# Performance work log

Hardware: AMD Instinct MI355X
Metric: run time of the kernel (lower is better)

Reference implementation:

```python
import jax, jax.numpy as jnp
import numpy as np

B, L, DM, DS, DC, E = 2, 1024, 1024, 16, 4, 2
DI = E * DM          # d_inner = 2048
DR = DM // 16        # dt_rank = 64
EPS = 1e-5


def setup_inputs() -> dict:
    key = jax.random.key(0)
    ks = jax.random.split(key, 8)
    s = lambda k, shp, sc: jax.random.normal(k, shp, jnp.float32) * sc
    return {
        "x": s(ks[0], (B, L, DM), 1.0),
        "norm_w": jnp.ones((DM,), jnp.float32),
        "in_proj_w": s(ks[1], (2 * DI, DM), 0.02),
        "conv_w": s(ks[2], (DI, 1, DC), 0.1),        # depthwise kernel [O=DI, I=1, W=DC]
        "conv_b": s(ks[3], (DI,), 0.02),
        "x_proj_w": s(ks[4], (DR + 2 * DS, DI), 0.02),
        "dt_proj_w": s(ks[5], (DI, DR), 0.02),
        "dt_proj_b": s(ks[6], (DI,), 0.02),
        "A_log": jnp.log(jnp.broadcast_to(jnp.arange(1, DS + 1, dtype=jnp.float32), (DI, DS))),
        "D": jnp.ones((DI,), jnp.float32),
        "out_proj_w": s(ks[7], (DM, DI), 0.02),
    }


def reference(x, norm_w, in_proj_w, conv_w, conv_b, x_proj_w,
              dt_proj_w, dt_proj_b, A_log, D, out_proj_w):
    # RMSNorm
    u = x * jax.lax.rsqrt(jnp.mean(x * x, axis=-1, keepdims=True) + EPS) * norm_w

    # in_proj -> [B, L, 2*DI], split into ssm branch and gate
    xz = jnp.einsum('bld,ed->ble', u, in_proj_w)
    xin, z = jnp.split(xz, 2, axis=-1)

    # causal depthwise conv along L + SiLU
    xc = jnp.transpose(xin, (0, 2, 1))                      # [B, DI, L]
    xc = jnp.pad(xc, ((0, 0), (0, 0), (DC - 1, 0)))
    xc = jax.lax.conv_general_dilated(xc, conv_w, (1,), 'VALID',
                                      feature_group_count=DI)  # [B, DI, L]
    xc = jax.nn.silu(xc + conv_b[None, :, None])
    xc = jnp.transpose(xc, (0, 2, 1))                       # [B, L, DI]

    # input-dependent dt, B, C
    dbl = jnp.einsum('bld,ed->ble', xc, x_proj_w)           # [B, L, DR+2*DS]
    dt, Bm, Cm = jnp.split(dbl, [DR, DR + DS], axis=-1)
    delta = jax.nn.softplus(jnp.einsum('blr,dr->bld', dt, dt_proj_w) + dt_proj_b)  # [B,L,DI]

    A = -jnp.exp(A_log)                                     # [DI, DS]
    dA = jnp.exp(delta[..., None] * A)                      # [B, L, DI, DS]
    dBu = delta[..., None] * Bm[:, :, None, :] * xc[..., None]  # [B, L, DI, DS]

    # selective scan: h_t = dA_t * h_{t-1} + dBu_t ; y_t = <h_t, C_t>
    def step(h, inp):
        da, dbu, c = inp
        h = da * h + dbu                                    # [B, DI, DS]
        return h, jnp.einsum('bdn,bn->bd', h, c)

    h0 = jnp.zeros((B, DI, DS), x.dtype)
    _, ys = jax.lax.scan(step, h0,
                         (jnp.swapaxes(dA, 0, 1),
                          jnp.swapaxes(dBu, 0, 1),
                          jnp.swapaxes(Cm, 0, 1)))
    y = jnp.swapaxes(ys, 0, 1) + xc * D                     # [B, L, DI]

    out = jnp.einsum('bld,ed->ble', y * jax.nn.silu(z), out_proj_w)
    return out + x  # residual
```

## Files before the change

### kernel.cpp

```cpp
#include <hip/hip_runtime.h>
#include <math.h>

#define B_   2
#define L_   1024
#define DM   1024
#define DS   16
#define DC   4
#define DI   2048
#define DR   64
#define NTOK (B_*L_)
#define EPSF 1e-5f
#define NC   32
#define CL   (L_/NC)
#define SPLITS 8

typedef __bf16 bf16_t;
typedef bf16_t bf16x4 __attribute__((ext_vector_type(4)));
typedef bf16_t bf16x8 __attribute__((ext_vector_type(8)));
typedef float  f32x4  __attribute__((ext_vector_type(4)));

__device__ __forceinline__ float siluf(float x){ return x / (1.f + __expf(-x)); }
__device__ __forceinline__ float softplusf(float x){ return (x > 20.f) ? x : log1pf(__expf(x)); }

__device__ __forceinline__ void gload_lds16(const void* g, void* l) {
    __builtin_amdgcn_global_load_lds(
        (const __attribute__((address_space(1))) void*)g,
        (__attribute__((address_space(3))) void*)l, 16, 0, 0);
}

struct hl_t { bf16_t h, l; };
__device__ __forceinline__ hl_t split2(float v) {
    hl_t r;
    r.h = (bf16_t)v;
    r.l = (bf16_t)(v - (float)r.h);
    return r;
}

#define SPLIT_IN_BLKS  ((2*DI*DM/4)/256)
#define SPLIT_X_BLKS   ((128*DI/4)/256)
#define SPLIT_O_BLKS   ((DM*DI/4)/256)
__global__ __launch_bounds__(256) void rms_split_all(
    const float* __restrict__ x, const float* __restrict__ w,
    bf16_t* __restrict__ uh, bf16_t* __restrict__ ul,
    const float* __restrict__ in_w, bf16_t* __restrict__ wih, bf16_t* __restrict__ wil,
    const float* __restrict__ x_w,  bf16_t* __restrict__ wxh,  bf16_t* __restrict__ wxl,
    const float* __restrict__ out_w, bf16_t* __restrict__ woh, bf16_t* __restrict__ wol)
{
    __shared__ float sred[4];
    int blk = blockIdx.x;
    int t = threadIdx.x;

    if (blk < NTOK) {
        int row = blk;
        float4 v = ((const float4*)(x + (size_t)row*DM))[t];
        float ss = v.x*v.x + v.y*v.y + v.z*v.z + v.w*v.w;
        #pragma unroll
        for (int off = 32; off > 0; off >>= 1) ss += __shfl_xor(ss, off, 64);
        if ((t & 63) == 0) sred[t >> 6] = ss;
        __syncthreads();
        ss = sred[0] + sred[1] + sred[2] + sred[3];
        float rs = rsqrtf(ss * (1.f/(float)DM) + EPSF);
        float4 wv = ((const float4*)w)[t];
        float o[4];
        o[0] = v.x*rs*wv.x; o[1] = v.y*rs*wv.y; o[2] = v.z*rs*wv.z; o[3] = v.w*rs*wv.w;
        bf16x4 hv, lv;
        #pragma unroll
        for (int j = 0; j < 4; ++j) { hl_t s = split2(o[j]); hv[j] = s.h; lv[j] = s.l; }
        *(bf16x4*)(uh + (size_t)row*DM + t*4) = hv;
        *(bf16x4*)(ul + (size_t)row*DM + t*4) = lv;
        return;
    }
    blk -= NTOK;
    if (blk < SPLIT_IN_BLKS) {
        int i = blk * 256 + t;
        float4 v = ((const float4*)in_w)[i];
        float o[4] = {v.x, v.y, v.z, v.w};
        bf16x4 hv, lv;
        #pragma unroll
        for (int j = 0; j < 4; ++j) { hl_t s = split2(o[j]); hv[j] = s.h; lv[j] = s.l; }
        ((bf16x4*)wih)[i] = hv;
        ((bf16x4*)wil)[i] = lv;
        return;
    }
    blk -= SPLIT_IN_BLKS;
    if (blk < SPLIT_X_BLKS) {
        int i = blk * 256 + t;
        int row = i >> 9;
        bf16x4 hv, lv;
        if (row < 96) {
            float4 v = ((const float4*)x_w)[i];
            float o[4] = {v.x, v.y, v.z, v.w};
            #pragma unroll
            for (int j = 0; j < 4; ++j) { hl_t s = split2(o[j]); hv[j] = s.h; lv[j] = s.l; }
        } else {
            #pragma unroll
            for (int j = 0; j < 4; ++j) { hv[j] = (bf16_t)0.f; lv[j] = (bf16_t)0.f; }
        }
        ((bf16x4*)wxh)[i] = hv;
        ((bf16x4*)wxl)[i] = lv;
        return;
    }
    blk -= SPLIT_X_BLKS;
    {
        int i = blk * 256 + t;
        float4 v = ((const float4*)out_w)[i];
        float o[4] = {v.x, v.y, v.z, v.w};
        bf16x4 hv, lv;
        #pragma unroll
        for (int j = 0; j < 4; ++j) { hl_t s = split2(o[j]); hv[j] = s.h; lv[j] = s.l; }
        ((bf16x4*)woh)[i] = hv;
        ((bf16x4*)wol)[i] = lv;
    }
}

template<int BN, int EPI, bool SK>
__global__ __launch_bounds__(256) void gemm_mfma(
    const bf16_t* __restrict__ Ah, const bf16_t* __restrict__ Al,
    const bf16_t* __restrict__ Bh, const bf16_t* __restrict__ Bl,
    float* __restrict__ C, int ldc,
    const float* __restrict__ res,
    int M, int N, int K, int kspl)
{
    constexpr int NJ   = BN / 32;
    constexpr int WN   = BN / 2;
    constexpr int ACH  = 8;
    constexpr int BCH  = BN / 16;
    constexpr int NCH  = 2*ACH + 2*BCH;
    constexpr int PERW = NCH / 4;
    constexpr int AOFF_L = 128*32;
    constexpr int BOFF_H = 2*128*32;
    constexpr int BOFF_L = 2*128*32 + BN*32;
    constexpr int BUFSZ  = 2*128*32 + 2*BN*32;

    __shared__ bf16_t lds[2*BUFSZ];

    int t = threadIdx.x;
    int w = t >> 6, lane = t & 63;
    int wr = w >> 1, wc = w & 1;

    int bx, by;
    if (!SK) {
        int bid = blockIdx.y * gridDim.x + blockIdx.x;
        int xcd = bid & 7;
        int i   = bid >> 3;
        bx = xcd * (int)(gridDim.x >> 3) + (i >> 4);
        by = i & 15;
    } else { bx = blockIdx.x; by = blockIdx.y; }

    int m0 = by * 128;
    int n0 = SK ? 0 : bx * BN;
    int k0beg = SK ? bx * kspl : 0;
    int nst = (SK ? kspl : K) >> 5;
    float* Cp = C;
    if (SK) Cp += (size_t)bx * M * BN;

    f32x4 acc[4][NJ];
    #pragma unroll
    for (int i = 0; i < 4; ++i)
        #pragma unroll
        for (int j = 0; j < NJ; ++j)
            acc[i][j] = (f32x4){0.f, 0.f, 0.f, 0.f};

    int lrow = lane >> 2;
    int lcol = (lane & 3) * 8;
    int ar   = wr*64 + (lane & 15);
    int br   = wc*WN + (lane & 15);
    int koff = (lane >> 4) * 8;

    auto STAGE = [&](int buf, int k0) {
        int base = buf ? BUFSZ : 0;
        #pragma unroll
        for (int q = 0; q < PERW; ++q) {
            int ch = w * PERW + q;
            const bf16_t* g; int le;
            if (ch < ACH) {
                int cc = ch;
                g  = Ah + (size_t)(m0 + cc*16 + lrow)*K + k0 + lcol;
                le = cc*512 + lane*8;
            } else if (ch < 2*ACH) {
                int cc = ch - ACH;
                g  = Al + (size_t)(m0 + cc*16 + lrow)*K + k0 + lcol;
                le = AOFF_L + cc*512 + lane*8;
            } else if (ch < 2*ACH + BCH) {
                int cc = ch - 2*ACH;
                g  = Bh + (size_t)(n0 + cc*16 + lrow)*K + k0 + lcol;
                le = BOFF_H + cc*512 + lane*8;
            } else {
                int cc = ch - 2*ACH - BCH;
                g  = Bl + (size_t)(n0 + cc*16 + lrow)*K + k0 + lcol;
                le = BOFF_L + cc*512 + lane*8;
            }
            gload_lds16(g, &lds[base + le]);
        }
    };

    STAGE(0, k0beg);
    __syncthreads();
    int cur = 0;
    for (int s = 0; s < nst; ++s) {
        int k0 = k0beg + (s << 5);
        if (s + 1 < nst) STAGE(cur ^ 1, k0 + 32);
        int base = cur ? BUFSZ : 0;

        bf16x8 ah[4], al4[4], bh[NJ], bl4[NJ];
        #pragma unroll
        for (int i = 0; i < 4; ++i) {
            ah[i]  = *(const bf16x8*)&lds[base + (ar + i*16)*32 + koff];
            al4[i] = *(const bf16x8*)&lds[base + AOFF_L + (ar + i*16)*32 + koff];
        }
        #pragma unroll
        for (int j = 0; j < NJ; ++j) {
            bh[j]  = *(const bf16x8*)&lds[base + BOFF_H + (br + j*16)*32 + koff];
            bl4[j] = *(const bf16x8*)&lds[base + BOFF_L + (br + j*16)*32 + koff];
        }
        #pragma unroll
        for (int i = 0; i < 4; ++i)
            #pragma unroll
            for (int j = 0; j < NJ; ++j) {
                acc[i][j] = __builtin_amdgcn_mfma_f32_16x16x32_bf16(ah[i],  bh[j],  acc[i][j], 0, 0, 0);
                acc[i][j] = __builtin_amdgcn_mfma_f32_16x16x32_bf16(al4[i], bh[j],  acc[i][j], 0, 0, 0);
                acc[i][j] = __builtin_amdgcn_mfma_f32_16x16x32_bf16(ah[i],  bl4[j], acc[i][j], 0, 0, 0);
            }
        __syncthreads();
        cur ^= 1;
    }

    int rb = m0 + wr*64 + (lane >> 4)*4;
    int cb = n0 + wc*WN + (lane & 15);
    #pragma unroll
    for (int i = 0; i < 4; ++i)
        #pragma unroll
        for (int j = 0; j < NJ; ++j) {
            int col = cb + j*16;
            #pragma unroll
            for (int r = 0; r < 4; ++r) {
                int row = rb + i*16 + r;
                float v = acc[i][j][r];
                if (EPI == 2) v += res[(size_t)row*ldc + col];
                Cp[(size_t)row*ldc + col] = v;
            }
        }
}

__global__ __launch_bounds__(256) void dt_fuse(
    const float* __restrict__ parts,
    float* __restrict__ bc,
    const float* __restrict__ dt_w,
    const float* __restrict__ dt_b,
    float* __restrict__ delta)
{
    __shared__ float dtsh[4][DR];
    int blk = blockIdx.x;
    int hf  = blk & 1;
    int tb  = blk >> 1;
    int t = threadIdx.x;
    if (t < 128) {
        int token = t >> 5;
        int c = (t & 31) * 4;
        int m = tb*4 + token;
        float4 s = {0.f, 0.f, 0.f, 0.f};
        #pragma unroll
        for (int sp = 0; sp < SPLITS; ++sp) {
            float4 v = *(const float4*)(parts + ((size_t)sp*NTOK + m)*128 + c);
            s.x += v.x; s.y += v.y; s.z += v.z; s.w += v.w;
        }
        if (c < 64) {
            *(float4*)&dtsh[token][c] = s;
        } else if (c < 96 && hf == 0) {
            *(float4*)(bc + (size_t)m*32 + (c - 64)) = s;
        }
    }
    __syncthreads();
    for (int dd = 0; dd < 4; ++dd) {
        int d = hf*1024 + dd*256 + t;
        const float4* wp = (const float4*)(dt_w + (size_t)d*DR);
        float bb = dt_b[d];
        float a0 = bb, a1 = bb, a2 = bb, a3 = bb;
        #pragma unroll 4
        for (int k4 = 0; k4 < 16; ++k4) {
            float4 wv = wp[k4];
            a0 = fmaf(wv.x, dtsh[0][k4*4+0], a0);
            a1 = fmaf(wv.x, dtsh[1][k4*4+0], a1);
            a2 = fmaf(wv.x, dtsh[2][k4*4+0], a2);
            a3 = fmaf(wv.x, dtsh[3][k4*4+0], a3);
            a0 = fmaf(wv.y, dtsh[0][k4*4+1], a0);
            a1 = fmaf(wv.y, dtsh[1][k4*4+1], a1);
            a2 = fmaf(wv.y, dtsh[2][k4*4+1], a2);
            a3 = fmaf(wv.y, dtsh[3][k4*4+1], a3);
            a0 = fmaf(wv.z, dtsh[0][k4*4+2], a0);
            a1 = fmaf(wv.z, dtsh[1][k4*4+2], a1);
            a2 = fmaf(wv.z, dtsh[2][k4*4+2], a2);
            a3 = fmaf(wv.z, dtsh[3][k4*4+2], a3);
            a0 = fmaf(wv.w, dtsh[0][k4*4+3], a0);
            a1 = fmaf(wv.w, dtsh[1][k4*4+3], a1);
            a2 = fmaf(wv.w, dtsh[2][k4*4+3], a2);
            a3 = fmaf(wv.w, dtsh[3][k4*4+3], a3);
        }
        delta[(size_t)(tb*4 + 0)*DI + d] = softplusf(a0);
        delta[(size_t)(tb*4 + 1)*DI + d] = softplusf(a1);
        delta[(size_t)(tb*4 + 2)*DI + d] = softplusf(a2);
        delta[(size_t)(tb*4 + 3)*DI + d] = softplusf(a3);
    }
}

__global__ __launch_bounds__(256) void conv_silu_k(const float* __restrict__ xz,
                                                   const float* __restrict__ cw,
                                                   const float* __restrict__ cb,
                                                   bf16_t* __restrict__ xch,
                                                   bf16_t* __restrict__ xcl)
{
    int idx = blockIdx.x * 256 + threadIdx.x;
    int d4 = idx & (DI/4 - 1);
    int m  = idx >> 9;
    int l  = m & (L_ - 1);
    int d  = d4 * 4;

    float4 w0 = *(const float4*)(cw + (size_t)(d+0)*DC);
    float4 w1 = *(const float4*)(cw + (size_t)(d+1)*DC);
    float4 w2 = *(const float4*)(cw + (size_t)(d+2)*DC);
    float4 w3 = *(const float4*)(cw + (size_t)(d+3)*DC);
    float wr0[4] = {w0.x,w0.y,w0.z,w0.w};
    float wr1[4] = {w1.x,w1.y,w1.z,w1.w};
    float wr2[4] = {w2.x,w2.y,w2.z,w2.w};
    float wr3[4] = {w3.x,w3.y,w3.z,w3.w};
    float4 bias = *(const float4*)(cb + d);
    float a0 = bias.x, a1 = bias.y, a2 = bias.z, a3 = bias.w;

    #pragma unroll
    for (int j = 0; j < DC; ++j) {
        int tt = l - (DC-1) + j;
        if (tt < 0) continue;
        float4 xv = *(const float4*)(xz + (size_t)(m - l + tt)*(2*DI) + d);
        a0 = fmaf(wr0[j], xv.x, a0);
        a1 = fmaf(wr1[j], xv.y, a1);
        a2 = fmaf(wr2[j], xv.z, a2);
        a3 = fmaf(wr3[j], xv.w, a3);
    }
    float o[4] = { siluf(a0), siluf(a1), siluf(a2), siluf(a3) };
    bf16x4 hv, lv;
    #pragma unroll
    for (int j = 0; j < 4; ++j) { hl_t s = split2(o[j]); hv[j] = s.h; lv[j] = s.l; }
    *(bf16x4*)(xch + (size_t)m*DI + d) = hv;
    *(bf16x4*)(xcl + (size_t)m*DI + d) = lv;
}

__global__ __launch_bounds__(256) void scan_p1(const float* __restrict__ delta,
                                               const bf16_t* __restrict__ xch,
                                               const bf16_t* __restrict__ xcl,
                                               const float* __restrict__ bc,
                                               const float* __restrict__ A_log,
                                               float* __restrict__ Sbuf,
                                               float* __restrict__ Hbuf)
{
    __shared__ float Bsh[CL][16];
    int t = threadIdx.x;
    int blk = blockIdx.x;
    int d = (blk & 7) * 256 + t;
    int c = (blk >> 3) & (NC - 1);
    int b = blk >> 8;
    int m0 = b * L_ + c * CL;

    for (int i = t; i < CL*16; i += 256)
        Bsh[i >> 4][i & 15] = bc[(size_t)(m0 + (i >> 4))*32 + (i & 15)];
    __syncthreads();

    float A[16], h[16];
    #pragma unroll
    for (int j = 0; j < 4; ++j) {
        float4 al = *(const float4*)(A_log + (size_t)d*DS + j*4);
        A[j*4+0] = -__expf(al.x); A[j*4+1] = -__expf(al.y);
        A[j*4+2] = -__expf(al.z); A[j*4+3] = -__expf(al.w);
    }
    #pragma unroll
    for (int n = 0; n < 16; ++n) h[n] = 0.f;
    float S = 0.f;

    #pragma unroll 4
    for (int tt = 0; tt < CL; ++tt) {
        int m = m0 + tt;
        float dv = delta[(size_t)m*DI + d];
        float xv = (float)xch[(size_t)m*DI + d] + (float)xcl[(size_t)m*DI + d];
        float dx = dv * xv;
        S += dv;
        #pragma unroll
        for (int n = 0; n < 16; ++n) {
            float dA = __expf(dv * A[n]);
            h[n] = fmaf(dA, h[n], Bsh[tt][n] * dx);
        }
    }

    Sbuf[(size_t)(b*NC + c)*DI + d] = S;
    size_t o = ((size_t)((b*NC + c)*DI) + d) * DS;
    #pragma unroll
    for (int j = 0; j < 4; ++j) {
        float4 hv;
        hv.x = h[j*4+0]; hv.y = h[j*4+1]; hv.z = h[j*4+2]; hv.w = h[j*4+3];
        *(float4*)(Hbuf + o + j*4) = hv;
    }
}

__global__ __launch_bounds__(256) void scan_p3(const float* __restrict__ delta,
                                               const float* __restrict__ xz,
                                               const bf16_t* __restrict__ xch,
                                               const bf16_t* __restrict__ xcl,
                                               const float* __restrict__ bc,
                                               const float* __restrict__ A_log,
                                               const float* __restrict__ Dp,
                                               const float* __restrict__ Sbuf,
                                               const float* __restrict__ Hbuf,
                                               bf16_t* __restrict__ gh,
                                               bf16_t* __restrict__ gl)
{
    __shared__ float Bsh[CL][16];
    __shared__ float Csh[CL][16];
    int t = threadIdx.x;
    int blk = blockIdx.x;
    int d = (blk & 7) * 256 + t;
    int c = (blk >> 3) & (NC - 1);
    int b = blk >> 8;
    int m0 = b * L_ + c * CL;

    for (int i = t; i < CL*16; i += 256) {
        int tt = i >> 4, n = i & 15;
        size_t ro = (size_t)(m0 + tt)*32;
        Bsh[tt][n] = bc[ro + n];
        Csh[tt][n] = bc[ro + 16 + n];
    }
    __syncthreads();

    float A[16], h[16];
    #pragma unroll
    for (int j = 0; j < 4; ++j) {
        float4 al = *(const float4*)(A_log + (size_t)d*DS + j*4);
        A[j*4+0] = -__expf(al.x); A[j*4+1] = -__expf(al.y);
        A[j*4+2] = -__expf(al.z); A[j*4+3] = -__expf(al.w);
    }
    #pragma unroll
    for (int n = 0; n < 16; ++n) h[n] = 0.f;
    for (int j = 0; j < c; ++j) {
        size_t so = (size_t)(b*NC + j)*DI + d;
        float S = Sbuf[so];
        size_t o = so * DS;
        float Hj[16];
        #pragma unroll
        for (int q = 0; q < 4; ++q) {
            float4 hv = *(const float4*)(Hbuf + o + q*4);
            Hj[q*4+0] = hv.x; Hj[q*4+1] = hv.y; Hj[q*4+2] = hv.z; Hj[q*4+3] = hv.w;
        }
        #pragma unroll
        for (int n = 0; n < 16; ++n)
            h[n] = fmaf(__expf(A[n]*S), h[n], Hj[n]);
    }
    float Dreg = Dp[d];

    for (int t0 = 0; t0 < CL; t0 += 4) {
        float dv[4], xv[4], zv[4];
        #pragma unroll
        for (int q = 0; q < 4; ++q) {
            int m = m0 + t0 + q;
            dv[q] = delta[(size_t)m*DI + d];
            xv[q] = (float)xch[(size_t)m*DI + d] + (float)xcl[(size_t)m*DI + d];
            zv[q] = xz[(size_t)m*(2*DI) + DI + d];
        }
        #pragma unroll
        for (int q = 0; q < 4; ++q) {
            int tt = t0 + q, m = m0 + tt;
            float dx = dv[q] * xv[q];
            float y = 0.f;
            #pragma unroll
            for (int n = 0; n < 16; ++n) {
                float dA = __expf(dv[q] * A[n]);
                h[n] = fmaf(dA, h[n], Bsh[tt][n] * dx);
                y = fmaf(h[n], Csh[tt][n], y);
            }
            float gv = (y + xv[q]*Dreg) * siluf(zv[q]);
            hl_t s = split2(gv);
            gh[(size_t)m*DI + d] = s.h;
            gl[(size_t)m*DI + d] = s.l;
        }
    }
}

extern "C" void kernel_launch(void* const* d_in, const int* in_sizes, int n_in,
                              void* d_out, int out_size, void* d_ws, size_t ws_size,
                              hipStream_t stream)
{
    const float* x         = (const float*)d_in[0];
    const float* norm_w    = (const float*)d_in[1];
    const float* in_proj_w = (const float*)d_in[2];
    const float* conv_w    = (const float*)d_in[3];
    const float* conv_b    = (const float*)d_in[4];
    const float* x_proj_w  = (const float*)d_in[5];
    const float* dt_proj_w = (const float*)d_in[6];
    const float* dt_proj_b = (const float*)d_in[7];
    const float* A_log     = (const float*)d_in[8];
    const float* Dp        = (const float*)d_in[9];
    const float* out_proj_w= (const float*)d_in[10];
    float* out = (float*)d_out;

    char* p = (char*)d_ws;
    float*  xz    = (float*)p;  p += (size_t)NTOK*2*DI*4;
    bf16_t* xch   = (bf16_t*)p; p += (size_t)NTOK*DI*2;
    bf16_t* xcl   = (bf16_t*)p; p += (size_t)NTOK*DI*2;
    float*  delta = (float*)p;  p += (size_t)NTOK*DI*4;
    float*  bc    = (float*)p;  p += (size_t)NTOK*32*4;
    float*  Hbuf  = (float*)p;  p += (size_t)B_*NC*DI*DS*4;
    char*   Wreg  = p;          p += (size_t)2*DI*DM*2*2;
    bf16_t* woh   = (bf16_t*)p; p += (size_t)DM*DI*2;
    bf16_t* wol   = (bf16_t*)p; p += (size_t)DM*DI*2;
    float*  Sbuf  = (float*)p;  p += (size_t)B_*NC*DI*4;
    bf16_t* wxh   = (bf16_t*)p; p += (size_t)128*DI*2;
    bf16_t* wxl   = (bf16_t*)p; p += (size_t)128*DI*2;

    bf16_t* uh  = (bf16_t*)Hbuf;
    bf16_t* ul  = uh + (size_t)NTOK*DM;
    float*  parts = Hbuf;
    bf16_t* wih = (bf16_t*)Wreg;
    bf16_t* wil = wih + (size_t)2*DI*DM;
    bf16_t* gh  = (bf16_t*)Wreg;
    bf16_t* gl  = gh + (size_t)NTOK*DI;

    rms_split_all<<<NTOK + SPLIT_IN_BLKS + SPLIT_X_BLKS + SPLIT_O_BLKS, 256, 0, stream>>>(
        x, norm_w, uh, ul, in_proj_w, wih, wil, x_proj_w, wxh, wxl,
        out_proj_w, woh, wol);

    gemm_mfma<128,0,false><<<dim3((2*DI)/128, NTOK/128), 256, 0, stream>>>(
        uh, ul, wih, wil, xz, 2*DI, nullptr, NTOK, 2*DI, DM, 0);

    conv_silu_k<<<(NTOK*(DI/4))/256, 256, 0, stream>>>(xz, conv_w, conv_b, xch, xcl);

    gemm_mfma<128,0,true><<<dim3(SPLITS, NTOK/128), 256, 0, stream>>>(
        xch, xcl, wxh, wxl, parts, 128, nullptr, NTOK, 128, DI, DI/SPLITS);

    dt_fuse<<<(NTOK/4)*2, 256, 0, stream>>>(parts, bc, dt_proj_w, dt_proj_b, delta);

    scan_p1<<<B_*NC*(DI/256), 256, 0, stream>>>(delta, xch, xcl, bc, A_log, Sbuf, Hbuf);
    scan_p3<<<B_*NC*(DI/256), 256, 0, stream>>>(delta, xz, xch, xcl, bc, A_log, Dp,
                                                Sbuf, Hbuf, gh, gl);

    gemm_mfma<64,2,false><<<dim3(DM/64, NTOK/128), 256, 0, stream>>>(
        gh, gl, woh, wol, out, DM, x, NTOK, DM, DI, 0);
}
```

Before: 320.6 us.

## Drop weight low-part bf16 split and add split-K to out projection

Weights are now converted to a single bf16 value instead of a high/low pair, so each GEMM issues two MFMAs per tile instead of three and stages less data in LDS. The output projection GEMM is split in two along K to double its grid, writing partial sums into the delta buffer. A new reduce kernel adds the two partials and the residual. This cuts MFMA work and weight conversion traffic, at the cost of lower weight precision, an extra kernel launch and more partial-sum memory traffic.

```diff
diff --git a/kernel.cpp b/kernel.cpp
--- a/kernel.cpp
+++ b/kernel.cpp
@@ -42,9 +42,9 @@
 __global__ __launch_bounds__(256) void rms_split_all(
     const float* __restrict__ x, const float* __restrict__ w,
     bf16_t* __restrict__ uh, bf16_t* __restrict__ ul,
-    const float* __restrict__ in_w, bf16_t* __restrict__ wih, bf16_t* __restrict__ wil,
-    const float* __restrict__ x_w,  bf16_t* __restrict__ wxh,  bf16_t* __restrict__ wxl,
-    const float* __restrict__ out_w, bf16_t* __restrict__ woh, bf16_t* __restrict__ wol)
+    const float* __restrict__ in_w, bf16_t* __restrict__ wih,
+    const float* __restrict__ x_w,  bf16_t* __restrict__ wxh,
+    const float* __restrict__ out_w, bf16_t* __restrict__ woh)
 {
     __shared__ float sred[4];
     int blk = blockIdx.x;
@@ -74,63 +74,52 @@
     if (blk < SPLIT_IN_BLKS) {
         int i = blk * 256 + t;
         float4 v = ((const float4*)in_w)[i];
-        float o[4] = {v.x, v.y, v.z, v.w};
-        bf16x4 hv, lv;
-        #pragma unroll
-        for (int j = 0; j < 4; ++j) { hl_t s = split2(o[j]); hv[j] = s.h; lv[j] = s.l; }
+        bf16x4 hv;
+        hv[0]=(bf16_t)v.x; hv[1]=(bf16_t)v.y; hv[2]=(bf16_t)v.z; hv[3]=(bf16_t)v.w;
         ((bf16x4*)wih)[i] = hv;
-        ((bf16x4*)wil)[i] = lv;
         return;
     }
     blk -= SPLIT_IN_BLKS;
     if (blk < SPLIT_X_BLKS) {
         int i = blk * 256 + t;
         int row = i >> 9;
-        bf16x4 hv, lv;
+        bf16x4 hv;
         if (row < 96) {
             float4 v = ((const float4*)x_w)[i];
-            float o[4] = {v.x, v.y, v.z, v.w};
-            #pragma unroll
-            for (int j = 0; j < 4; ++j) { hl_t s = split2(o[j]); hv[j] = s.h; lv[j] = s.l; }
+            hv[0]=(bf16_t)v.x; hv[1]=(bf16_t)v.y; hv[2]=(bf16_t)v.z; hv[3]=(bf16_t)v.w;
         } else {
             #pragma unroll
-            for (int j = 0; j < 4; ++j) { hv[j] = (bf16_t)0.f; lv[j] = (bf16_t)0.f; }
+            for (int j = 0; j < 4; ++j) hv[j] = (bf16_t)0.f;
         }
         ((bf16x4*)wxh)[i] = hv;
-        ((bf16x4*)wxl)[i] = lv;
         return;
     }
     blk -= SPLIT_X_BLKS;
     {
         int i = blk * 256 + t;
         float4 v = ((const float4*)out_w)[i];
-        float o[4] = {v.x, v.y, v.z, v.w};
-        bf16x4 hv, lv;
-        #pragma unroll
-        for (int j = 0; j < 4; ++j) { hl_t s = split2(o[j]); hv[j] = s.h; lv[j] = s.l; }
+        bf16x4 hv;
+        hv[0]=(bf16_t)v.x; hv[1]=(bf16_t)v.y; hv[2]=(bf16_t)v.z; hv[3]=(bf16_t)v.w;
         ((bf16x4*)woh)[i] = hv;
-        ((bf16x4*)wol)[i] = lv;
-    }
-}
-
-template<int BN, int EPI, bool SK>
+    }
+}
+
+template<int BN, int MODE>
 __global__ __launch_bounds__(256) void gemm_mfma(
     const bf16_t* __restrict__ Ah, const bf16_t* __restrict__ Al,
-    const bf16_t* __restrict__ Bh, const bf16_t* __restrict__ Bl,
+    const bf16_t* __restrict__ Bh,
     float* __restrict__ C, int ldc,
-    const float* __restrict__ res,
     int M, int N, int K, int kspl)
 {
     constexpr int NJ   = BN / 32;
     constexpr int WN   = BN / 2;
     constexpr int ACH  = 8;
     constexpr int BCH  = BN / 16;
-    constexpr int NCH  = 2*ACH + 2*BCH;
+    constexpr int NCH  = 2*ACH + BCH;
     constexpr int PERW = NCH / 4;
     constexpr int AOFF_L = 128*32;
     constexpr int BOFF_H = 2*128*32;
-    constexpr int BOFF_L = 2*128*32 + BN*32;
-    constexpr int BUFSZ  = 2*128*32 + 2*BN*32;
+    constexpr int BUFSZ  = 2*128*32 + BN*32;
 
     __shared__ bf16_t lds[2*BUFSZ];
 
@@ -138,21 +127,30 @@
     int w = t >> 6, lane = t & 63;
     int wr = w >> 1, wc = w & 1;
 
-    int bx, by;
-    if (!SK) {
+    int m0, n0, k0beg;
+    float* Cp = C;
+    if (MODE == 0) {
         int bid = blockIdx.y * gridDim.x + blockIdx.x;
         int xcd = bid & 7;
         int i   = bid >> 3;
-        bx = xcd * (int)(gridDim.x >> 3) + (i >> 4);
-        by = i & 15;
-    } else { bx = blockIdx.x; by = blockIdx.y; }
-
-    int m0 = by * 128;
-    int n0 = SK ? 0 : bx * BN;
-    int k0beg = SK ? bx * kspl : 0;
-    int nst = (SK ? kspl : K) >> 5;
-    float* Cp = C;
-    if (SK) Cp += (size_t)bx * M * BN;
+        int bx = xcd * (int)(gridDim.x >> 3) + (i >> 4);
+        m0 = (i & 15) * 128;
+        n0 = bx * BN;
+        k0beg = 0;
+    } else if (MODE == 1) {
+        m0 = blockIdx.y * 128;
+        n0 = 0;
+        k0beg = blockIdx.x * kspl;
+        Cp += (size_t)blockIdx.x * M * BN;
+    } else {
+        int ntile = blockIdx.x & 15;
+        int split = blockIdx.x >> 4;
+        m0 = blockIdx.y * 128;
+        n0 = ntile * BN;
+        k0beg = split * kspl;
+        Cp += (size_t)split * M * N;
+    }
+    int nst = ((MODE == 0) ? K : kspl) >> 5;
 
     f32x4 acc[4][NJ];
     #pragma unroll
@@ -181,14 +179,10 @@
                 int cc = ch - ACH;
                 g  = Al + (size_t)(m0 + cc*16 + lrow)*K + k0 + lcol;
                 le = AOFF_L + cc*512 + lane*8;
-            } else if (ch < 2*ACH + BCH) {
+            } else {
                 int cc = ch - 2*ACH;
                 g  = Bh + (size_t)(n0 + cc*16 + lrow)*K + k0 + lcol;
                 le = BOFF_H + cc*512 + lane*8;
-            } else {
-                int cc = ch - 2*ACH - BCH;
-                g  = Bl + (size_t)(n0 + cc*16 + lrow)*K + k0 + lcol;
-                le = BOFF_L + cc*512 + lane*8;
             }
             gload_lds16(g, &lds[base + le]);
         }
@@ -202,24 +196,21 @@
         if (s + 1 < nst) STAGE(cur ^ 1, k0 + 32);
         int base = cur ? BUFSZ : 0;
 
-        bf16x8 ah[4], al4[4], bh[NJ], bl4[NJ];
+        bf16x8 ah[4], al4[4], bh[NJ];
         #pragma unroll
         for (int i = 0; i < 4; ++i) {
             ah[i]  = *(const bf16x8*)&lds[base + (ar + i*16)*32 + koff];
             al4[i] = *(const bf16x8*)&lds[base + AOFF_L + (ar + i*16)*32 + koff];
         }
         #pragma unroll
-        for (int j = 0; j < NJ; ++j) {
+        for (int j = 0; j < NJ; ++j)
             bh[j]  = *(const bf16x8*)&lds[base + BOFF_H + (br + j*16)*32 + koff];
-            bl4[j] = *(const bf16x8*)&lds[base + BOFF_L + (br + j*16)*32 + koff];
-        }
         #pragma unroll
         for (int i = 0; i < 4; ++i)
             #pragma unroll
             for (int j = 0; j < NJ; ++j) {
-                acc[i][j] = __builtin_amdgcn_mfma_f32_16x16x32_bf16(ah[i],  bh[j],  acc[i][j], 0, 0, 0);
-                acc[i][j] = __builtin_amdgcn_mfma_f32_16x16x32_bf16(al4[i], bh[j],  acc[i][j], 0, 0, 0);
-                acc[i][j] = __builtin_amdgcn_mfma_f32_16x16x32_bf16(ah[i],  bl4[j], acc[i][j], 0, 0, 0);
+                acc[i][j] = __builtin_amdgcn_mfma_f32_16x16x32_bf16(ah[i],  bh[j], acc[i][j], 0, 0, 0);
+                acc[i][j] = __builtin_amdgcn_mfma_f32_16x16x32_bf16(al4[i], bh[j], acc[i][j], 0, 0, 0);
             }
         __syncthreads();
         cur ^= 1;
@@ -235,11 +226,24 @@
             #pragma unroll
             for (int r = 0; r < 4; ++r) {
                 int row = rb + i*16 + r;
-                float v = acc[i][j][r];
-                if (EPI == 2) v += res[(size_t)row*ldc + col];
-                Cp[(size_t)row*ldc + col] = v;
+                Cp[(size_t)row*ldc + col] = acc[i][j][r];
             }
         }
+}
+
+__global__ __launch_bounds__(256) void reduce_out(
+    const float* __restrict__ parts,
+    const float* __restrict__ x,
+    float* __restrict__ out)
+{
+    int i = blockIdx.x * 256 + threadIdx.x;
+    float4 a = ((const float4*)parts)[i];
+    float4 b = ((const float4*)(parts + (size_t)NTOK*DM))[i];
+    float4 xv = ((const float4*)x)[i];
+    float4 o;
+    o.x = a.x + b.x + xv.x; o.y = a.y + b.y + xv.y;
+    o.z = a.z + b.z + xv.z; o.w = a.w + b.w + xv.w;
+    ((float4*)out)[i] = o;
 }
 
 __global__ __launch_bounds__(256) void dt_fuse(
@@ -505,32 +509,29 @@
     float*  delta = (float*)p;  p += (size_t)NTOK*DI*4;
     float*  bc    = (float*)p;  p += (size_t)NTOK*32*4;
     float*  Hbuf  = (float*)p;  p += (size_t)B_*NC*DI*DS*4;
-    char*   Wreg  = p;          p += (size_t)2*DI*DM*2*2;
+    char*   Wreg  = p;          p += (size_t)2*DI*DM*2;
+    bf16_t* gl    = (bf16_t*)p; p += (size_t)NTOK*DI*2;
     bf16_t* woh   = (bf16_t*)p; p += (size_t)DM*DI*2;
-    bf16_t* wol   = (bf16_t*)p; p += (size_t)DM*DI*2;
     float*  Sbuf  = (float*)p;  p += (size_t)B_*NC*DI*4;
     bf16_t* wxh   = (bf16_t*)p; p += (size_t)128*DI*2;
-    bf16_t* wxl   = (bf16_t*)p; p += (size_t)128*DI*2;
 
     bf16_t* uh  = (bf16_t*)Hbuf;
     bf16_t* ul  = uh + (size_t)NTOK*DM;
     float*  parts = Hbuf;
     bf16_t* wih = (bf16_t*)Wreg;
-    bf16_t* wil = wih + (size_t)2*DI*DM;
     bf16_t* gh  = (bf16_t*)Wreg;
-    bf16_t* gl  = gh + (size_t)NTOK*DI;
+    float*  oparts = delta;
 
     rms_split_all<<<NTOK + SPLIT_IN_BLKS + SPLIT_X_BLKS + SPLIT_O_BLKS, 256, 0, stream>>>(
-        x, norm_w, uh, ul, in_proj_w, wih, wil, x_proj_w, wxh, wxl,
-        out_proj_w, woh, wol);
-
-    gemm_mfma<128,0,false><<<dim3((2*DI)/128, NTOK/128), 256, 0, stream>>>(
-        uh, ul, wih, wil, xz, 2*DI, nullptr, NTOK, 2*DI, DM, 0);
+        x, norm_w, uh, ul, in_proj_w, wih, x_proj_w, wxh, out_proj_w, woh);
+
+    gemm_mfma<128,0><<<dim3((2*DI)/128, NTOK/128), 256, 0, stream>>>(
+        uh, ul, wih, xz, 2*DI, NTOK, 2*DI, DM, 0);
 
     conv_silu_k<<<(NTOK*(DI/4))/256, 256, 0, stream>>>(xz, conv_w, conv_b, xch, xcl);
 
-    gemm_mfma<128,0,true><<<dim3(SPLITS, NTOK/128), 256, 0, stream>>>(
-        xch, xcl, wxh, wxl, parts, 128, nullptr, NTOK, 128, DI, DI/SPLITS);
+    gemm_mfma<128,1><<<dim3(SPLITS, NTOK/128), 256, 0, stream>>>(
+        xch, xcl, wxh, parts, 128, NTOK, 128, DI, DI/SPLITS);
 
     dt_fuse<<<(NTOK/4)*2, 256, 0, stream>>>(parts, bc, dt_proj_w, dt_proj_b, delta);
 
@@ -538,6 +539,8 @@
     scan_p3<<<B_*NC*(DI/256), 256, 0, stream>>>(delta, xz, xch, xcl, bc, A_log, Dp,
                                                 Sbuf, Hbuf, gh, gl);
 
-    gemm_mfma<64,2,false><<<dim3(DM/64, NTOK/128), 256, 0, stream>>>(
-        gh, gl, woh, wol, out, DM, x, NTOK, DM, DI, 0);
-}
+    gemm_mfma<64,2><<<dim3(32, NTOK/128), 256, 0, stream>>>(
+        gh, gl, woh, oparts, DM, NTOK, DM, DI, DI/2);
+
+    reduce_out<<<(NTOK*DM/4)/256, 256, 0, stream>>>(oparts, x, out);
+}
```

New measurement: 292.2 us. 1.1x faster.
